# Kernel optimization log

Measured on AMD Instinct MI355X. Metric: run time of the kernel, lower is better.

## Reference

```python
import jax, jax.numpy as jnp
import numpy as np

B, M, E, K = 2048, 768, 16384, 32
EPS = 1e-8  # torch F.cosine_similarity default eps


def setup_inputs() -> dict:
    key = jax.random.key(0)
    ks = jax.random.split(key, 13)
    s_m = 1.0 / np.sqrt(M)  # nn.Linear(M, E) init bound
    s_e = 1.0 / np.sqrt(E)  # nn.Linear(E, M) init bound
    u = lambda k, shape, s: jax.random.uniform(k, shape, jnp.float32, -s, s)
    return {
        "x": jax.random.normal(ks[0], (B, M), jnp.float32),
        "enc_w": u(ks[1], (E, M), s_m), "enc_b": u(ks[2], (E,), s_m),
        "dec_w": u(ks[3], (M, E), s_e), "dec_b": u(ks[4], (M,), s_e),
        "enc1_w": u(ks[5], (E, M), s_m), "enc1_b": u(ks[6], (E,), s_m),
        "dec1_w": u(ks[7], (M, E), s_e), "dec1_b": u(ks[8], (M,), s_e),
        "enc2_w": u(ks[9], (E, M), s_m), "enc2_b": u(ks[10], (E,), s_m),
        "dec2_w": u(ks[11], (M, E), s_e), "dec2_b": u(ks[12], (M,), s_e),
        "k": K,
    }


def _aux_loss(a_BE, win_BE, c1_BE, c2_BE, dp_ME, d1_ME, d2_ME):
    # Faithful reduction of the B x M x E cosine-similarity along M:
    #   scaled_parent[b,:,e] = dp[:,e]*a[b,e];  scaled_child uses d1/d2 per winner mask.
    # cos_sim needs only M-dim dot products / norms of decoder columns.
    np2_E = jnp.sum(dp_ME * dp_ME, axis=0)   # ||dp_e||^2
    n1_E = jnp.sum(d1_ME * d1_ME, axis=0)
    n2_E = jnp.sum(d2_ME * d2_ME, axis=0)
    dp1_E = jnp.sum(dp_ME * d1_ME, axis=0)   # <dp_e, d1_e>
    dp2_E = jnp.sum(dp_ME * d2_ME, axis=0)
    c_BE = jnp.where(win_BE, c1_BE, c2_BE)
    dpc_BE = jnp.where(win_BE, dp1_E, dp2_E)
    nc_BE = jnp.where(win_BE, n1_E, n2_E)
    a2 = a_BE * a_BE
    dot = a2 * np2_E + a_BE * c_BE * dpc_BE                      # <parent, parent+child>
    norm_p = jnp.abs(a_BE) * jnp.sqrt(np2_E)                     # ||parent||
    comb2 = a2 * np2_E + 2.0 * a_BE * c_BE * dpc_BE + c_BE * c_BE * nc_BE
    norm_c = jnp.sqrt(jnp.maximum(comb2, 0.0))                   # ||parent+child||
    cos = dot / (jnp.maximum(norm_p, EPS) * jnp.maximum(norm_c, EPS))
    active = a_BE > 0
    return -jnp.sum(jnp.where(active, cos, 0.0)) / a_BE.shape[0]


def reference(x, enc_w, enc_b, dec_w, dec_b, enc1_w, enc1_b, dec1_w, dec1_b,
              enc2_w, enc2_b, dec2_w, dec2_b, k):
    Bn = x.shape[0]
    En = enc_w.shape[0]
    pre_BE = x @ enc_w.T + enc_b
    vals, idx = jax.lax.top_k(pre_BE, k)                         # [B,k]
    sae_BE = jnp.zeros_like(pre_BE).at[jnp.arange(Bn)[:, None], idx].set(vals)
    num_live_parent = jnp.zeros((En,), bool).at[idx.ravel()].set(True).sum()

    pre1_BE = x @ enc1_w.T + enc1_b
    pre2_BE = x @ enc2_w.T + enc2_b
    active = sae_BE != 0.0
    m1_BE = jnp.where(active, pre1_BE, 0.0)
    m2_BE = jnp.where(active, pre2_BE, 0.0)
    win_BE = m1_BE > m2_BE
    f1_BE = jnp.where(win_BE, m1_BE, 0.0)
    f2_BE = jnp.where(~win_BE, m2_BE, 0.0)
    num_live_c1 = jnp.any(f1_BE != 0, axis=0).sum()
    num_live_c2 = jnp.any(f2_BE != 0, axis=0).sum()

    recon_BM = (sae_BE @ dec_w.T + dec_b) + (f1_BE @ dec1_w.T + dec1_b) + (f2_BE @ dec2_w.T + dec2_b)

    sg = jax.lax.stop_gradient
    aux = _aux_loss(sg(sae_BE), sg(win_BE), sg(f1_BE), sg(f2_BE), dec_w, dec1_w, dec2_w)
    return recon_BM, (num_live_parent, num_live_c1, num_live_c2), aux
```

## Files before the change

### kernel.cpp

```cpp
#include <hip/hip_runtime.h>
#include <cstdint>
#include <cstddef>

#define B_N 2048
#define M_N 768
#define E_N 16384
#define K_N 32
#define EPSF 1e-8f

typedef __attribute__((ext_vector_type(8))) short short8;
typedef __attribute__((ext_vector_type(4))) float floatx4;
typedef __attribute__((ext_vector_type(4))) unsigned short ushort4v;

__device__ inline unsigned short f2bf(float f) {
  unsigned int u = __float_as_uint(f);
  unsigned int r = (u + 0x7fffu + ((u >> 16) & 1u)) >> 16;
  return (unsigned short)r;
}
__device__ inline float bf2f(unsigned short h) {
  return __uint_as_float(((unsigned int)h) << 16);
}

__global__ __launch_bounds__(256) void split2_kernel(
    const float* __restrict__ inA, unsigned short* __restrict__ hiA,
    unsigned short* __restrict__ loA, int n4A,
    const float* __restrict__ inB, unsigned short* __restrict__ hiB,
    unsigned short* __restrict__ loB, int n4B) {
  int i = blockIdx.x * 256 + threadIdx.x;
  const float* in;
  unsigned short* hi;
  unsigned short* lo;
  int idx;
  if (i < n4A) {
    in = inA; hi = hiA; lo = loA; idx = i;
  } else {
    idx = i - n4A;
    if (idx >= n4B) return;
    in = inB; hi = hiB; lo = loB;
  }
  float4 v = ((const float4*)in)[idx];
  ushort4v h, l;
  h.x = f2bf(v.x); l.x = f2bf(v.x - bf2f(h.x));
  h.y = f2bf(v.y); l.y = f2bf(v.y - bf2f(h.y));
  h.z = f2bf(v.z); l.z = f2bf(v.z - bf2f(h.z));
  h.w = f2bf(v.w); l.w = f2bf(v.w - bf2f(h.w));
  ((ushort4v*)hi)[idx] = h;
  ((ushort4v*)lo)[idx] = l;
}

__global__ __launch_bounds__(256) void prep_dec_kernel(
    const float* __restrict__ dw, const float* __restrict__ d1,
    const float* __restrict__ d2,
    float* __restrict__ dT0, float* __restrict__ dT1,
    float* __restrict__ dT2, float* __restrict__ stats) {
  __shared__ float t0[32][36], t1[32][36], t2[32][36];
  int tid = threadIdx.x;
  int e0 = blockIdx.x * 32;
  int m0 = blockIdx.y * 32;

  {
    int ml = tid >> 3, e4 = tid & 7;
    size_t gbase = (size_t)(m0 + ml) * E_N + e0 + e4 * 4;
    float4 a  = *(const float4*)&dw[gbase];
    float4 b1 = *(const float4*)&d1[gbase];
    float4 b2 = *(const float4*)&d2[gbase];
    *(float4*)&t0[ml][e4 * 4] = a;
    *(float4*)&t1[ml][e4 * 4] = b1;
    *(float4*)&t2[ml][e4 * 4] = b2;
  }
  __syncthreads();

  int el = tid >> 3, m4 = tid & 7;
  float4 v0, v1, v2;
  float s0 = 0.f, s1 = 0.f, s2 = 0.f, s3 = 0.f, s4 = 0.f;
#pragma unroll
  for (int j = 0; j < 4; ++j) {
    float A  = t0[m4 * 4 + j][el];
    float B1 = t1[m4 * 4 + j][el];
    float B2 = t2[m4 * 4 + j][el];
    ((float*)&v0)[j] = A;
    ((float*)&v1)[j] = B1;
    ((float*)&v2)[j] = B2;
    s0 = fmaf(A, A, s0);
    s1 = fmaf(B1, B1, s1);
    s2 = fmaf(B2, B2, s2);
    s3 = fmaf(A, B1, s3);
    s4 = fmaf(A, B2, s4);
  }
  size_t tbase = (size_t)(e0 + el) * M_N + m0 + m4 * 4;
  *(float4*)&dT0[tbase] = v0;
  *(float4*)&dT1[tbase] = v1;
  *(float4*)&dT2[tbase] = v2;

#pragma unroll
  for (int off = 1; off < 8; off <<= 1) {
    s0 += __shfl_xor(s0, off);
    s1 += __shfl_xor(s1, off);
    s2 += __shfl_xor(s2, off);
    s3 += __shfl_xor(s3, off);
    s4 += __shfl_xor(s4, off);
  }
  if (m4 == 0) {
    int e = e0 + el;
    atomicAdd(&stats[e], s0);
    atomicAdd(&stats[E_N + e], s1);
    atomicAdd(&stats[2 * E_N + e], s2);
    atomicAdd(&stats[3 * E_N + e], s3);
    atomicAdd(&stats[4 * E_N + e], s4);
  }
}

#define TM 128
#define TN 128
#define TK 32
#define LDK 40

__global__ __launch_bounds__(256) void gemm_mfma_kernel(
    const unsigned short* __restrict__ Ahi, const unsigned short* __restrict__ Alo,
    const unsigned short* __restrict__ Bhi, const unsigned short* __restrict__ Blo,
    const float* __restrict__ bias, float* __restrict__ C) {
  __shared__ __align__(16) unsigned short As_hi[TM * LDK];
  __shared__ __align__(16) unsigned short As_lo[TM * LDK];
  __shared__ __align__(16) unsigned short Bs_hi[TM * LDK];
  __shared__ __align__(16) unsigned short Bs_lo[TM * LDK];

  int tid = threadIdx.x;
  int lane = tid & 63;
  int wave = tid >> 6;
  int i0 = blockIdx.y * TM;
  int j0 = blockIdx.x * TN;
  int wm = (wave >> 1) * 64;
  int wn = (wave & 1) * 64;

  int row0 = tid >> 2, c40 = tid & 3;
  int row1 = 64 + (tid >> 2), c41 = tid & 3;
  const unsigned short* pAhi0 = Ahi + (size_t)(i0 + row0) * M_N + c40 * 8;
  const unsigned short* pAhi1 = Ahi + (size_t)(i0 + row1) * M_N + c41 * 8;
  const unsigned short* pAlo0 = Alo + (size_t)(i0 + row0) * M_N + c40 * 8;
  const unsigned short* pAlo1 = Alo + (size_t)(i0 + row1) * M_N + c41 * 8;
  const unsigned short* pBhi0 = Bhi + (size_t)(j0 + row0) * M_N + c40 * 8;
  const unsigned short* pBhi1 = Bhi + (size_t)(j0 + row1) * M_N + c41 * 8;
  const unsigned short* pBlo0 = Blo + (size_t)(j0 + row0) * M_N + c40 * 8;
  const unsigned short* pBlo1 = Blo + (size_t)(j0 + row1) * M_N + c41 * 8;
  int l0 = row0 * LDK + c40 * 8;
  int l1 = row1 * LDK + c41 * 8;

  floatx4 acc[4][4];
#pragma unroll
  for (int i = 0; i < 4; ++i)
#pragma unroll
    for (int j = 0; j < 4; ++j) acc[i][j] = (floatx4){0.f, 0.f, 0.f, 0.f};

  int fr = lane & 15;
  int fk = (lane >> 4) * 8;

  short8 vAh0 = *(const short8*)pAhi0;
  short8 vAh1 = *(const short8*)pAhi1;
  short8 vAl0 = *(const short8*)pAlo0;
  short8 vAl1 = *(const short8*)pAlo1;
  short8 vBh0 = *(const short8*)pBhi0;
  short8 vBh1 = *(const short8*)pBhi1;
  short8 vBl0 = *(const short8*)pBlo0;
  short8 vBl1 = *(const short8*)pBlo1;

  for (int k0 = 0; k0 < M_N; k0 += TK) {
    __syncthreads();
    *(short8*)&As_hi[l0] = vAh0;
    *(short8*)&As_hi[l1] = vAh1;
    *(short8*)&As_lo[l0] = vAl0;
    *(short8*)&As_lo[l1] = vAl1;
    *(short8*)&Bs_hi[l0] = vBh0;
    *(short8*)&Bs_hi[l1] = vBh1;
    *(short8*)&Bs_lo[l0] = vBl0;
    *(short8*)&Bs_lo[l1] = vBl1;
    __syncthreads();

    if (k0 + TK < M_N) {
      int d = k0 + TK;
      vAh0 = *(const short8*)(pAhi0 + d);
      vAh1 = *(const short8*)(pAhi1 + d);
      vAl0 = *(const short8*)(pAlo0 + d);
      vAl1 = *(const short8*)(pAlo1 + d);
      vBh0 = *(const short8*)(pBhi0 + d);
      vBh1 = *(const short8*)(pBhi1 + d);
      vBl0 = *(const short8*)(pBlo0 + d);
      vBl1 = *(const short8*)(pBlo1 + d);
    }

    short8 ah[4], al[4], bh[4], bl[4];
#pragma unroll
    for (int t = 0; t < 4; ++t) {
      int ar = (wm + t * 16 + fr) * LDK + fk;
      int br = (wn + t * 16 + fr) * LDK + fk;
      ah[t] = *(const short8*)&As_hi[ar];
      al[t] = *(const short8*)&As_lo[ar];
      bh[t] = *(const short8*)&Bs_hi[br];
      bl[t] = *(const short8*)&Bs_lo[br];
    }
#pragma unroll
    for (int mi = 0; mi < 4; ++mi)
#pragma unroll
      for (int ni = 0; ni < 4; ++ni) {
        acc[mi][ni] = __builtin_amdgcn_mfma_f32_16x16x32_bf16(ah[mi], bh[ni], acc[mi][ni], 0, 0, 0);
        acc[mi][ni] = __builtin_amdgcn_mfma_f32_16x16x32_bf16(ah[mi], bl[ni], acc[mi][ni], 0, 0, 0);
        acc[mi][ni] = __builtin_amdgcn_mfma_f32_16x16x32_bf16(al[mi], bh[ni], acc[mi][ni], 0, 0, 0);
      }
  }

#pragma unroll
  for (int mi = 0; mi < 4; ++mi) {
    int rbase = i0 + wm + mi * 16 + (lane >> 4) * 4;
#pragma unroll
    for (int ni = 0; ni < 4; ++ni) {
      int col = j0 + wn + ni * 16 + (lane & 15);
      float bb = bias[col];
#pragma unroll
      for (int r = 0; r < 4; ++r) {
        C[(size_t)(rbase + r) * E_N + col] = acc[mi][ni][r] + bb;
      }
    }
  }
}

__global__ __launch_bounds__(256) void topk_kernel(const float* __restrict__ pre,
                                                   int* __restrict__ topk_idx,
                                                   float* __restrict__ topk_val,
                                                   int* __restrict__ live_p) {
  int b = blockIdx.x;
  int tid = threadIdx.x;
  int wave = tid >> 6;
  const float* row = pre + (size_t)b * E_N;

  __shared__ __align__(16) unsigned int hist4[4][2048];
  __shared__ unsigned int csum[256];
  __shared__ float candV[2048];
  __shared__ int candI[2048];
  __shared__ float defV[K_N];
  __shared__ int defI[K_N];
  __shared__ int s_T, s_nDef, s_nCand;

  uint4 z4 = make_uint4(0u, 0u, 0u, 0u);
  uint4* hz = (uint4*)&hist4[0][0];
  for (int i = tid; i < 2048; i += 256) hz[i] = z4;
  if (tid == 0) { s_nDef = 0; s_nCand = 0; }
  __syncthreads();

  for (int j = 0; j < E_N / 1024; ++j) {
    float4 v = ((const float4*)row)[tid + j * 256];
    float f[4] = {v.x, v.y, v.z, v.w};
#pragma unroll
    for (int q = 0; q < 4; ++q) {
      unsigned int u = __float_as_uint(f[q]);
      unsigned int key = (u & 0x80000000u) ? ~u : (u | 0x80000000u);
      atomicAdd(&hist4[wave][key >> 21], 1u);
    }
  }
  __syncthreads();

  unsigned int hm[8];
#pragma unroll
  for (int i = 0; i < 8; ++i) hm[i] = 0u;
#pragma unroll
  for (int w = 0; w < 4; ++w) {
    uint4 p0 = *(const uint4*)&hist4[w][tid * 8];
    uint4 p1 = *(const uint4*)&hist4[w][tid * 8 + 4];
    hm[0] += p0.x; hm[1] += p0.y; hm[2] += p0.z; hm[3] += p0.w;
    hm[4] += p1.x; hm[5] += p1.y; hm[6] += p1.z; hm[7] += p1.w;
  }
  unsigned int sc = hm[0] + hm[1] + hm[2] + hm[3] + hm[4] + hm[5] + hm[6] + hm[7];
  csum[tid] = sc;
  __syncthreads();
  for (int off = 1; off < 256; off <<= 1) {
    unsigned int v_ = (tid + off < 256) ? csum[tid + off] : 0u;
    __syncthreads();
    csum[tid] += v_;
    __syncthreads();
  }
  {
    unsigned int above = (tid < 255) ? csum[tid + 1] : 0u;
    if (csum[tid] >= K_N && above < K_N) {
      unsigned int run = above;
      int T = 0;
#pragma unroll
      for (int i = 7; i >= 0; --i) {
        run += hm[i];
        if (run >= K_N) { T = tid * 8 + i; break; }
      }
      s_T = T;
    }
  }
  __syncthreads();
  int T = s_T;

  for (int j = 0; j < E_N / 1024; ++j) {
    int i4 = tid + j * 256;
    float4 v = ((const float4*)row)[i4];
    float f[4] = {v.x, v.y, v.z, v.w};
#pragma unroll
    for (int q = 0; q < 4; ++q) {
      float vv = f[q];
      unsigned int u = __float_as_uint(vv);
      unsigned int key = (u & 0x80000000u) ? ~u : (u | 0x80000000u);
      int bk = key >> 21;
      if (bk > T) {
        int d = atomicAdd(&s_nDef, 1);
        defV[d] = vv;
        defI[d] = i4 * 4 + q;
      } else if (bk == T) {
        int c = atomicAdd(&s_nCand, 1);
        candV[c] = vv;
        candI[c] = i4 * 4 + q;
      }
    }
  }
  __syncthreads();
  int nDef = s_nDef;
  int nCand = s_nCand;
  int need = K_N - nDef;

  if (tid < nDef) {
    topk_idx[b * K_N + tid] = defI[tid];
    topk_val[b * K_N + tid] = defV[tid];
    live_p[defI[tid]] = 1;
  }
  for (int c = tid; c < nCand; c += 256) {
    float v = candV[c];
    int idx = candI[c];
    int r = 0;
    for (int j2 = 0; j2 < nCand; ++j2) {
      float vj = candV[j2];
      r += (vj > v) || (vj == v && candI[j2] < idx);
    }
    if (r < need) {
      int slot = nDef + r;
      topk_idx[b * K_N + slot] = idx;
      topk_val[b * K_N + slot] = v;
      live_p[idx] = 1;
    }
  }
}

__global__ __launch_bounds__(256, 6) void child_recon_kernel(
    const float* __restrict__ x, const float* __restrict__ e1w, const float* __restrict__ e1b,
    const float* __restrict__ e2w, const float* __restrict__ e2b,
    const int* __restrict__ topk_idx, const float* __restrict__ topk_val,
    int* __restrict__ live_c1, int* __restrict__ live_c2,
    const float* __restrict__ stats, float* __restrict__ aux_sum,
    const float* __restrict__ decT0, const float* __restrict__ decT1,
    const float* __restrict__ decT2,
    const float* __restrict__ db0, const float* __restrict__ db1,
    const float* __restrict__ db2, float* __restrict__ out) {
  int b = blockIdx.x;
  int tid = threadIdx.x;
  int lane = tid & 63;
  int wave = tid >> 6;

  __shared__ float xs[M_N];
  __shared__ int es[K_N];
  __shared__ float as[K_N], cs[K_N];
  __shared__ int wf[K_N];

  if (tid < K_N) {
    es[tid] = topk_idx[b * K_N + tid];
    as[tid] = topk_val[b * K_N + tid];
  }
  if (tid < M_N / 4) ((float4*)xs)[tid] = ((const float4*)(x + (size_t)b * M_N))[tid];
  __syncthreads();

#pragma unroll
  for (int it = 0; it < 4; ++it) {
    int sA = it * 8 + wave * 2;
    int sB = sA + 1;
    int eA = es[sA], eB = es[sB];
    float aA = as[sA], aB = as[sB];
    const float* w1A = e1w + (size_t)eA * M_N;
    const float* w2A = e2w + (size_t)eA * M_N;
    const float* w1B = e1w + (size_t)eB * M_N;
    const float* w2B = e2w + (size_t)eB * M_N;
    float d1A = 0.f, d2A = 0.f, d1B = 0.f, d2B = 0.f;
#pragma unroll
    for (int j = 0; j < 3; ++j) {
      int m = (lane << 2) + j * 256;
      float4 xv = *(const float4*)&xs[m];
      float4 a1 = *(const float4*)&w1A[m];
      float4 a2 = *(const float4*)&w2A[m];
      float4 b1 = *(const float4*)&w1B[m];
      float4 b2 = *(const float4*)&w2B[m];
      d1A += xv.x * a1.x + xv.y * a1.y + xv.z * a1.z + xv.w * a1.w;
      d2A += xv.x * a2.x + xv.y * a2.y + xv.z * a2.z + xv.w * a2.w;
      d1B += xv.x * b1.x + xv.y * b1.y + xv.z * b1.z + xv.w * b1.w;
      d2B += xv.x * b2.x + xv.y * b2.y + xv.z * b2.z + xv.w * b2.w;
    }
#pragma unroll
    for (int off = 32; off > 0; off >>= 1) {
      d1A += __shfl_down(d1A, off);
      d2A += __shfl_down(d2A, off);
      d1B += __shfl_down(d1B, off);
      d2B += __shfl_down(d2B, off);
    }
    if (lane == 0) {
#pragma unroll
      for (int h = 0; h < 2; ++h) {
        int s = h ? sB : sA;
        int e = h ? eB : eA;
        float a = h ? aB : aA;
        float d1 = h ? d1B : d1A;
        float d2 = h ? d2B : d2A;
        if (a != 0.f) {
          float m1 = d1 + e1b[e];
          float m2 = d2 + e2b[e];
          bool win = m1 > m2;
          float f1 = win ? m1 : 0.f;
          float f2 = win ? 0.f : m2;
          float c = win ? f1 : f2;
          cs[s] = c;
          wf[s] = win ? 1 : 0;
          if (f1 != 0.f) live_c1[e] = 1;
          if (f2 != 0.f) live_c2[e] = 1;
        } else {
          cs[s] = 0.f;
          wf[s] = 0;
        }
      }
    }
  }
  __syncthreads();

  float cosv = 0.f;
  if (tid < K_N) {
    float a = as[tid];
    if (a > 0.f) {
      int e = es[tid];
      float c = cs[tid];
      int win = wf[tid];
      float np2e = stats[e];
      float nce = win ? stats[E_N + e] : stats[2 * E_N + e];
      float dpc = win ? stats[3 * E_N + e] : stats[4 * E_N + e];
      float a2 = a * a;
      float dot = a2 * np2e + a * c * dpc;
      float normp = fabsf(a) * sqrtf(np2e);
      float comb2 = a2 * np2e + 2.f * a * c * dpc + c * c * nce;
      float normc = sqrtf(fmaxf(comb2, 0.f));
      cosv = dot / (fmaxf(normp, EPSF) * fmaxf(normc, EPSF));
    }
  }
  if (tid < 64) {
#pragma unroll
    for (int off = 32; off > 0; off >>= 1) cosv += __shfl_down(cosv, off);
    if (tid == 0) atomicAdd(aux_sum, cosv);
  }

  float acc0 = db0[tid] + db1[tid] + db2[tid];
  float acc1 = db0[tid + 256] + db1[tid + 256] + db2[tid + 256];
  float acc2 = db0[tid + 512] + db1[tid + 512] + db2[tid + 512];

#pragma unroll 4
  for (int s = 0; s < K_N; ++s) {
    int e = es[s];
    float a = as[s];
    float c = cs[s];
    const float* p = decT0 + (size_t)e * M_N;
    const float* q = (wf[s] ? decT1 : decT2) + (size_t)e * M_N;
    float p0 = p[tid], p1 = p[tid + 256], p2 = p[tid + 512];
    float q0 = q[tid], q1 = q[tid + 256], q2 = q[tid + 512];
    acc0 = fmaf(a, p0, fmaf(c, q0, acc0));
    acc1 = fmaf(a, p1, fmaf(c, q1, acc1));
    acc2 = fmaf(a, p2, fmaf(c, q2, acc2));
  }
  out[(size_t)b * M_N + tid] = acc0;
  out[(size_t)b * M_N + tid + 256] = acc1;
  out[(size_t)b * M_N + tid + 512] = acc2;
}

__global__ void finalize_kernel(const int* __restrict__ live_p, const int* __restrict__ live_c1,
                                const int* __restrict__ live_c2, const float* __restrict__ aux_sum,
                                float* __restrict__ out_tail) {
  int tid = threadIdx.x;
  int c0 = 0, c1 = 0, c2 = 0;
  for (int i = tid; i < E_N; i += 256) {
    c0 += live_p[i];
    c1 += live_c1[i];
    c2 += live_c2[i];
  }
  __shared__ int r0[256], r1[256], r2[256];
  r0[tid] = c0; r1[tid] = c1; r2[tid] = c2;
  __syncthreads();
  for (int s = 128; s > 0; s >>= 1) {
    if (tid < s) { r0[tid] += r0[tid + s]; r1[tid] += r1[tid + s]; r2[tid] += r2[tid + s]; }
    __syncthreads();
  }
  if (tid == 0) {
    out_tail[0] = (float)r0[0];
    out_tail[1] = (float)r1[0];
    out_tail[2] = (float)r2[0];
    out_tail[3] = -aux_sum[0] / (float)B_N;
  }
}

extern "C" void kernel_launch(void* const* d_in, const int* in_sizes, int n_in,
                              void* d_out, int out_size, void* d_ws, size_t ws_size,
                              hipStream_t stream) {
  const float* x     = (const float*)d_in[0];
  const float* enc_w = (const float*)d_in[1];
  const float* enc_b = (const float*)d_in[2];
  const float* dec_w = (const float*)d_in[3];
  const float* dec_b = (const float*)d_in[4];
  const float* e1w   = (const float*)d_in[5];
  const float* e1b   = (const float*)d_in[6];
  const float* d1w   = (const float*)d_in[7];
  const float* d1b   = (const float*)d_in[8];
  const float* e2w   = (const float*)d_in[9];
  const float* e2b   = (const float*)d_in[10];
  const float* d2w   = (const float*)d_in[11];
  const float* d2b   = (const float*)d_in[12];

  float* wsf = (float*)d_ws;

  const size_t PRE_F = (size_t)B_N * E_N;
  const size_t XSP_F = (size_t)B_N * M_N / 2;
  const size_t ESP_F = (size_t)E_N * M_N / 2;
  const size_t DEC_F = (size_t)E_N * M_N;
  const size_t BIG_F = PRE_F + 2 * XSP_F + 2 * ESP_F;

  float* pre = wsf;
  unsigned short* xhi  = (unsigned short*)(wsf + PRE_F);
  unsigned short* xlo  = (unsigned short*)(wsf + PRE_F + XSP_F);
  unsigned short* ewhi = (unsigned short*)(wsf + PRE_F + 2 * XSP_F);
  unsigned short* ewlo = (unsigned short*)(wsf + PRE_F + 2 * XSP_F + ESP_F);
  float* decT0 = wsf;
  float* decT1 = wsf + DEC_F;
  float* decT2 = wsf + 2 * DEC_F;

  size_t off = BIG_F;
  float* stats  = wsf + off;
  int*   livep  = (int*)(wsf + off + 5 * (size_t)E_N);
  int*   livec1 = livep + E_N;
  int*   livec2 = livep + 2 * E_N;
  float* auxs   = (float*)(livep + 3 * E_N);
  off += 8 * (size_t)E_N + 64;
  off &= ~(size_t)63;
  int*   tidx = (int*)(wsf + off);    off += (size_t)B_N * K_N;
  float* tval = wsf + off;            off += (size_t)B_N * K_N;

  hipMemsetAsync(stats, 0, (8 * (size_t)E_N + 1) * sizeof(float), stream);

  int n4A = B_N * M_N / 4;
  int n4B = E_N * M_N / 4;
  split2_kernel<<<(n4A + n4B + 255) / 256, 256, 0, stream>>>(x, xhi, xlo, n4A,
                                                             enc_w, ewhi, ewlo, n4B);

  const int HB = B_N / 2;
  gemm_mfma_kernel<<<dim3(E_N / TN, HB / TM), 256, 0, stream>>>(xhi, xlo, ewhi, ewlo, enc_b, pre);
  gemm_mfma_kernel<<<dim3(E_N / TN, HB / TM), 256, 0, stream>>>(
      xhi + (size_t)HB * M_N, xlo + (size_t)HB * M_N, ewhi, ewlo, enc_b,
      pre + (size_t)HB * E_N);

  topk_kernel<<<B_N, 256, 0, stream>>>(pre, tidx, tval, livep);

  prep_dec_kernel<<<dim3(E_N / 32, M_N / 32), 256, 0, stream>>>(
      dec_w, d1w, d2w, decT0, decT1, decT2, stats);

  float* out = (float*)d_out;
  child_recon_kernel<<<HB, 256, 0, stream>>>(x, e1w, e1b, e2w, e2b, tidx, tval,
                                             livec1, livec2, stats, auxs,
                                             decT0, decT1, decT2, dec_b, d1b, d2b, out);
  child_recon_kernel<<<HB, 256, 0, stream>>>(
      x + (size_t)HB * M_N, e1w, e1b, e2w, e2b, tidx + (size_t)HB * K_N,
      tval + (size_t)HB * K_N, livec1, livec2, stats, auxs,
      decT0, decT1, decT2, dec_b, d1b, d2b, out + (size_t)HB * M_N);

  finalize_kernel<<<1, 256, 0, stream>>>(livep, livec1, livec2, auxs,
                                         out + (size_t)B_N * M_N);
}
```

Baseline: 654.8 us.

## Enlarge decoder transpose tiles, cache top-k row in registers, merge split launches

The decoder transpose/stats kernel now uses 64x64 tiles instead of 32x32, so each thread does more work and issues fewer stat atomics per element. The top-k kernel loads each 16384-element row into 64 registers once and reuses them for both the histogram pass and the candidate pass, removing the second global read. The GEMM and child-recon kernels, previously launched twice over half batches, are now launched once over the full batch. The cost is higher register pressure in top-k (64 floats per thread), which may lower occupancy, and more LDS per block in the transpose kernel.

After: 613.8 us. 1.07x faster.

```diff
diff --git a/kernel.cpp b/kernel.cpp
--- a/kernel.cpp
+++ b/kernel.cpp
@@ -53,60 +53,66 @@
     const float* __restrict__ d2,
     float* __restrict__ dT0, float* __restrict__ dT1,
     float* __restrict__ dT2, float* __restrict__ stats) {
-  __shared__ float t0[32][36], t1[32][36], t2[32][36];
+  __shared__ float t0[64][68], t1[64][68], t2[64][68];
   int tid = threadIdx.x;
-  int e0 = blockIdx.x * 32;
-  int m0 = blockIdx.y * 32;
-
-  {
-    int ml = tid >> 3, e4 = tid & 7;
-    size_t gbase = (size_t)(m0 + ml) * E_N + e0 + e4 * 4;
-    float4 a  = *(const float4*)&dw[gbase];
-    float4 b1 = *(const float4*)&d1[gbase];
-    float4 b2 = *(const float4*)&d2[gbase];
-    *(float4*)&t0[ml][e4 * 4] = a;
-    *(float4*)&t1[ml][e4 * 4] = b1;
-    *(float4*)&t2[ml][e4 * 4] = b2;
-  }
-  __syncthreads();
-
-  int el = tid >> 3, m4 = tid & 7;
-  float4 v0, v1, v2;
-  float s0 = 0.f, s1 = 0.f, s2 = 0.f, s3 = 0.f, s4 = 0.f;
-#pragma unroll
-  for (int j = 0; j < 4; ++j) {
-    float A  = t0[m4 * 4 + j][el];
-    float B1 = t1[m4 * 4 + j][el];
-    float B2 = t2[m4 * 4 + j][el];
-    ((float*)&v0)[j] = A;
-    ((float*)&v1)[j] = B1;
-    ((float*)&v2)[j] = B2;
-    s0 = fmaf(A, A, s0);
-    s1 = fmaf(B1, B1, s1);
-    s2 = fmaf(B2, B2, s2);
-    s3 = fmaf(A, B1, s3);
-    s4 = fmaf(A, B2, s4);
-  }
-  size_t tbase = (size_t)(e0 + el) * M_N + m0 + m4 * 4;
-  *(float4*)&dT0[tbase] = v0;
-  *(float4*)&dT1[tbase] = v1;
-  *(float4*)&dT2[tbase] = v2;
-
-#pragma unroll
-  for (int off = 1; off < 8; off <<= 1) {
-    s0 += __shfl_xor(s0, off);
-    s1 += __shfl_xor(s1, off);
-    s2 += __shfl_xor(s2, off);
-    s3 += __shfl_xor(s3, off);
-    s4 += __shfl_xor(s4, off);
-  }
-  if (m4 == 0) {
-    int e = e0 + el;
-    atomicAdd(&stats[e], s0);
-    atomicAdd(&stats[E_N + e], s1);
-    atomicAdd(&stats[2 * E_N + e], s2);
-    atomicAdd(&stats[3 * E_N + e], s3);
-    atomicAdd(&stats[4 * E_N + e], s4);
+  int e0 = blockIdx.x * 64;
+  int m0 = blockIdx.y * 64;
+
+  int ml = tid >> 4, e4 = tid & 15;
+#pragma unroll
+  for (int r = 0; r < 64; r += 16) {
+    size_t g = (size_t)(m0 + ml + r) * E_N + e0 + e4 * 4;
+    *(float4*)&t0[ml + r][e4 * 4] = *(const float4*)&dw[g];
+    *(float4*)&t1[ml + r][e4 * 4] = *(const float4*)&d1[g];
+    *(float4*)&t2[ml + r][e4 * 4] = *(const float4*)&d2[g];
+  }
+  __syncthreads();
+
+  int m4 = tid & 7;
+  int elb = tid >> 3;
+#pragma unroll
+  for (int ee = 0; ee < 2; ++ee) {
+    int el = elb + ee * 32;
+    float s0 = 0.f, s1 = 0.f, s2 = 0.f, s3 = 0.f, s4 = 0.f;
+#pragma unroll
+    for (int jj = 0; jj < 2; ++jj) {
+      float4 v0, v1, v2;
+#pragma unroll
+      for (int j = 0; j < 4; ++j) {
+        int m = m4 * 4 + jj * 32 + j;
+        float A  = t0[m][el];
+        float B1 = t1[m][el];
+        float B2 = t2[m][el];
+        ((float*)&v0)[j] = A;
+        ((float*)&v1)[j] = B1;
+        ((float*)&v2)[j] = B2;
+        s0 = fmaf(A, A, s0);
+        s1 = fmaf(B1, B1, s1);
+        s2 = fmaf(B2, B2, s2);
+        s3 = fmaf(A, B1, s3);
+        s4 = fmaf(A, B2, s4);
+      }
+      size_t tb = (size_t)(e0 + el) * M_N + m0 + m4 * 4 + jj * 32;
+      *(float4*)&dT0[tb] = v0;
+      *(float4*)&dT1[tb] = v1;
+      *(float4*)&dT2[tb] = v2;
+    }
+#pragma unroll
+    for (int off = 1; off < 8; off <<= 1) {
+      s0 += __shfl_xor(s0, off);
+      s1 += __shfl_xor(s1, off);
+      s2 += __shfl_xor(s2, off);
+      s3 += __shfl_xor(s3, off);
+      s4 += __shfl_xor(s4, off);
+    }
+    if (m4 == 0) {
+      int e = e0 + el;
+      atomicAdd(&stats[e], s0);
+      atomicAdd(&stats[E_N + e], s1);
+      atomicAdd(&stats[2 * E_N + e], s2);
+      atomicAdd(&stats[3 * E_N + e], s3);
+      atomicAdd(&stats[4 * E_N + e], s4);
+    }
   }
 }
 
@@ -245,15 +251,21 @@
   if (tid == 0) { s_nDef = 0; s_nCand = 0; }
   __syncthreads();
 
-  for (int j = 0; j < E_N / 1024; ++j) {
+  float rv[64];
+#pragma unroll
+  for (int j = 0; j < 16; ++j) {
     float4 v = ((const float4*)row)[tid + j * 256];
-    float f[4] = {v.x, v.y, v.z, v.w};
-#pragma unroll
-    for (int q = 0; q < 4; ++q) {
-      unsigned int u = __float_as_uint(f[q]);
-      unsigned int key = (u & 0x80000000u) ? ~u : (u | 0x80000000u);
-      atomicAdd(&hist4[wave][key >> 21], 1u);
-    }
+    rv[4 * j + 0] = v.x;
+    rv[4 * j + 1] = v.y;
+    rv[4 * j + 2] = v.z;
+    rv[4 * j + 3] = v.w;
+  }
+
+#pragma unroll
+  for (int j = 0; j < 64; ++j) {
+    unsigned int u = __float_as_uint(rv[j]);
+    unsigned int key = (u & 0x80000000u) ? ~u : (u | 0x80000000u);
+    atomicAdd(&hist4[wave][key >> 21], 1u);
   }
   __syncthreads();
 
@@ -292,24 +304,22 @@
   __syncthreads();
   int T = s_T;
 
-  for (int j = 0; j < E_N / 1024; ++j) {
-    int i4 = tid + j * 256;
-    float4 v = ((const float4*)row)[i4];
-    float f[4] = {v.x, v.y, v.z, v.w};
-#pragma unroll
-    for (int q = 0; q < 4; ++q) {
-      float vv = f[q];
-      unsigned int u = __float_as_uint(vv);
-      unsigned int key = (u & 0x80000000u) ? ~u : (u | 0x80000000u);
-      int bk = key >> 21;
+#pragma unroll
+  for (int jj = 0; jj < 64; ++jj) {
+    float vv = rv[jj];
+    unsigned int u = __float_as_uint(vv);
+    unsigned int key = (u & 0x80000000u) ? ~u : (u | 0x80000000u);
+    int bk = key >> 21;
+    if (bk >= T) {
+      int idx = (tid + (jj >> 2) * 256) * 4 + (jj & 3);
       if (bk > T) {
         int d = atomicAdd(&s_nDef, 1);
         defV[d] = vv;
-        defI[d] = i4 * 4 + q;
-      } else if (bk == T) {
+        defI[d] = idx;
+      } else {
         int c = atomicAdd(&s_nCand, 1);
         candV[c] = vv;
-        candI[c] = i4 * 4 + q;
+        candI[c] = idx;
       }
     }
   }
@@ -549,25 +559,17 @@
   split2_kernel<<<(n4A + n4B + 255) / 256, 256, 0, stream>>>(x, xhi, xlo, n4A,
                                                              enc_w, ewhi, ewlo, n4B);
 
-  const int HB = B_N / 2;
-  gemm_mfma_kernel<<<dim3(E_N / TN, HB / TM), 256, 0, stream>>>(xhi, xlo, ewhi, ewlo, enc_b, pre);
-  gemm_mfma_kernel<<<dim3(E_N / TN, HB / TM), 256, 0, stream>>>(
-      xhi + (size_t)HB * M_N, xlo + (size_t)HB * M_N, ewhi, ewlo, enc_b,
-      pre + (size_t)HB * E_N);
+  gemm_mfma_kernel<<<dim3(E_N / TN, B_N / TM), 256, 0, stream>>>(xhi, xlo, ewhi, ewlo, enc_b, pre);
 
   topk_kernel<<<B_N, 256, 0, stream>>>(pre, tidx, tval, livep);
 
-  prep_dec_kernel<<<dim3(E_N / 32, M_N / 32), 256, 0, stream>>>(
+  prep_dec_kernel<<<dim3(E_N / 64, M_N / 64), 256, 0, stream>>>(
       dec_w, d1w, d2w, decT0, decT1, decT2, stats);
 
   float* out = (float*)d_out;
-  child_recon_kernel<<<HB, 256, 0, stream>>>(x, e1w, e1b, e2w, e2b, tidx, tval,
-                                             livec1, livec2, stats, auxs,
-                                             decT0, decT1, decT2, dec_b, d1b, d2b, out);
-  child_recon_kernel<<<HB, 256, 0, stream>>>(
-      x + (size_t)HB * M_N, e1w, e1b, e2w, e2b, tidx + (size_t)HB * K_N,
-      tval + (size_t)HB * K_N, livec1, livec2, stats, auxs,
-      decT0, decT1, decT2, dec_b, d1b, d2b, out + (size_t)HB * M_N);
+  child_recon_kernel<<<B_N, 256, 0, stream>>>(x, e1w, e1b, e2w, e2b, tidx, tval,
+                                              livec1, livec2, stats, auxs,
+                                              decT0, decT1, decT2, dec_b, d1b, d2b, out);
 
   finalize_kernel<<<1, 256, 0, stream>>>(livep, livec1, livec2, auxs,
                                          out + (size_t)B_N * M_N);
```
